# Optimization experiments

Measured on AMD Instinct MI355X. Metric: run time of the kernel, lower is better.

## Reference

```python
import jax, jax.numpy as jnp
import numpy as np

TOP_K = 50  # standard DND neighbourhood size
N_STEPS = 5


def _mlp(x, W1, b1, W2, b2, W3, b3):
    h = jax.nn.elu(x @ W1 + b1)
    h = jax.nn.elu(h @ W2 + b2)
    return h @ W3 + b3  # [B, 1]


def setup_inputs() -> dict:
    key = jax.random.key(0)
    ks = jax.random.split(key, 10)
    B, A, N, D = 1024, 5, 16384, 512
    return {
        "embeddings": jax.random.normal(ks[0], (B, D), jnp.float32),
        "keys": jax.random.normal(ks[1], (A, N, D), jnp.float32),
        "mem_values": jax.random.normal(ks[2], (A, N, D), jnp.float32),
        "W1": jax.random.normal(ks[3], (D, 256), jnp.float32) * 0.02,
        "b1": jnp.zeros((256,), jnp.float32),
        "W2": jax.random.normal(ks[4], (256, 128), jnp.float32) * 0.02,
        "b2": jnp.zeros((128,), jnp.float32),
        "W3": jax.random.normal(ks[5], (128, 1), jnp.float32) * 0.02,
        "b3": jnp.zeros((1,), jnp.float32),
        "actions": jax.random.randint(ks[6], (B, N_STEPS), 0, A, jnp.int32),
    }


def reference(embeddings, keys, mem_values, W1, b1, W2, b2, W3, b3, actions):
    # embeddings: [B, D]; keys/mem_values: [A, N, D]; actions: [B, 5]
    B, D = embeddings.shape
    eps = 1e-8
    # normalize memory keys once (cosine-similarity DND kernel)
    kn = keys / (jnp.linalg.norm(keys, axis=-1, keepdims=True) + eps)  # [A, N, D]

    def dnd_lookup_all(q):
        # q: [B, D] -> kNN-weighted readout from every action's memory: [A, B, D]
        qn = q / (jnp.linalg.norm(q, axis=-1, keepdims=True) + eps)
        sims = jnp.einsum("bd,and->abn", qn, kn)          # [A, B, N]
        s_k, idx = jax.lax.top_k(sims, TOP_K)             # [A, B, K]
        w = jax.nn.softmax(s_k, axis=-1)                  # [A, B, K]
        v_k = jax.vmap(lambda v, i: v[i])(mem_values, idx)  # [A, B, K, D]
        return jnp.einsum("abk,abkd->abd", w, v_k)

    pred_values = _mlp(embeddings, W1, b1, W2, b2, W3, b3)  # [B, 1]

    b_idx = jnp.arange(B)
    cur = embeddings
    step_vals = []
    for t in range(N_STEPS):
        out_all = dnd_lookup_all(cur)          # [A, B, D]
        cur = out_all[actions[:, t], b_idx]    # [B, D] per-sample action select
        step_vals.append(_mlp(cur, W1, b1, W2, b2, W3, b3))  # [B, 1]

    # original concatenates sample-major: [v1_i..v5_i] for each i -> [5B, 1]
    pred_nstep = jnp.stack(step_vals, axis=1).reshape(-1, 1)
    return jnp.concatenate([pred_values, pred_nstep], axis=0)  # [6B, 1]
```

## Files before the change

### kernel.cpp

```cpp
#include <hip/hip_runtime.h>

#define A_CNT   5
#define NB      1024
#define DIM     512
#define NMEM    16384
#define TOPK    50
#define NSTEPS  5
#define H1N     256
#define H2N     128

#define TM      128
#define TN      128
#define MSEL    100
#define RCAP    512

struct TileDesc { int a; int s0; int nvalid; int pad; };

typedef __bf16 bf16x8 __attribute__((ext_vector_type(8)));
typedef short  s16x8  __attribute__((ext_vector_type(8)));
typedef float  f32x4  __attribute__((ext_vector_type(4)));

template <typename T>
__device__ __forceinline__ auto mfma_try(T a, T b, f32x4 c, int)
    -> decltype(__builtin_amdgcn_mfma_f32_16x16x32_bf16(a, b, c, 0, 0, 0)) {
    return __builtin_amdgcn_mfma_f32_16x16x32_bf16(a, b, c, 0, 0, 0);
}
template <typename T>
__device__ __forceinline__ f32x4 mfma_try(T a, T b, f32x4 c, long) {
    return __builtin_amdgcn_mfma_f32_16x16x32_bf16(
        __builtin_bit_cast(s16x8, a), __builtin_bit_cast(s16x8, b), c, 0, 0, 0);
}
__device__ __forceinline__ f32x4 mfma_bf16(uint4 a, uint4 b, f32x4 c) {
    return mfma_try(__builtin_bit_cast(bf16x8, a), __builtin_bit_cast(bf16x8, b), c, 0);
}

union BF8 { bf16x8 v; uint4 u; };

__device__ __forceinline__ void gload_lds16(const void* g, void* l) {
    __builtin_amdgcn_global_load_lds(
        (const __attribute__((address_space(1))) void*)(unsigned long long)g,
        (__attribute__((address_space(3))) void*)(unsigned)(unsigned long long)l,
        16, 0, 0);
}

__global__ __launch_bounds__(256) void k_prep_keys(const float* __restrict__ keys,
                                                   float* __restrict__ inv,
                                                   unsigned short* __restrict__ kb) {
    int row  = blockIdx.x * 4 + (threadIdx.x >> 6);
    int lane = threadIdx.x & 63;
    const float* p = keys + (size_t)row * DIM;
    float ss = 0.f;
    for (int i = lane; i < DIM; i += 64) { float v = p[i]; ss += v * v; }
    for (int o = 32; o; o >>= 1) ss += __shfl_down(ss, o);
    ss = __shfl(ss, 0);
    if (lane == 0) inv[row] = 1.0f / (sqrtf(ss) + 1e-8f);
    const float4* s4 = (const float4*)(p + lane * 8);
    float4 v0 = s4[0], v1 = s4[1];
    BF8 pk;
    pk.v[0] = (__bf16)v0.x; pk.v[1] = (__bf16)v0.y;
    pk.v[2] = (__bf16)v0.z; pk.v[3] = (__bf16)v0.w;
    pk.v[4] = (__bf16)v1.x; pk.v[5] = (__bf16)v1.y;
    pk.v[6] = (__bf16)v1.z; pk.v[7] = (__bf16)v1.w;
    *(uint4*)(kb + (size_t)row * DIM + lane * 8) = pk.u;
}

__global__ __launch_bounds__(256) void k_qnorm(const float* __restrict__ x,
                                               float* __restrict__ qn,
                                               unsigned short* __restrict__ qb) {
    int row = blockIdx.x, tid = threadIdx.x;
    const float* p = x + (size_t)row * DIM;
    float ss = 0.f;
    for (int i = tid; i < DIM; i += 256) { float v = p[i]; ss += v * v; }
    for (int o = 32; o; o >>= 1) ss += __shfl_down(ss, o);
    __shared__ float w4[4];
    if ((tid & 63) == 0) w4[tid >> 6] = ss;
    __syncthreads();
    float tot = w4[0] + w4[1] + w4[2] + w4[3];
    float s = 1.0f / (sqrtf(tot) + 1e-8f);
    float* q = qn + (size_t)row * DIM;
    unsigned short* qbr = qb + (size_t)row * DIM;
    for (int i = tid; i < DIM; i += 256) {
        float v = p[i] * s;
        q[i] = v;
        __bf16 h = (__bf16)v;
        qbr[i] = __builtin_bit_cast(unsigned short, h);
    }
}

__global__ void k_group_all(const int* __restrict__ actions,
                            int* __restrict__ sorted_b_all, int* __restrict__ sorted_a_all,
                            TileDesc* __restrict__ descs_all, int cb, int maxd, int nch) {
    int t = blockIdx.x;
    int* sorted_b = sorted_b_all + t * NB;
    int* sorted_a = sorted_a_all + t * NB;
    TileDesc* descs = descs_all + t * (nch * maxd);
    int lane = threadIdx.x;
    for (int i = lane; i < nch * maxd; i += 64) descs[i].a = -1;
    __shared__ int gs[A_CNT + 1];
    int out_pos = 0;
    for (int a = 0; a < A_CNT; a++) {
        if (lane == 0) gs[a] = out_pos;
        for (int c = 0; c < NB; c += 64) {
            int b = c + lane;
            int act = actions[b * NSTEPS + t];
            unsigned long long m = __ballot(act == a);
            int rank = __popcll(m & ((1ULL << lane) - 1ULL));
            if (act == a) { sorted_b[out_pos + rank] = b; sorted_a[out_pos + rank] = a; }
            out_pos += __popcll(m);
        }
    }
    if (lane == 0) {
        gs[A_CNT] = NB;
        int ndc[4] = {0, 0, 0, 0};
        for (int a = 0; a < A_CNT; a++) {
            int s = gs[a], e = gs[a + 1];
            while (s < e) {
                int c = s / cb;
                int lim = min(e, (c + 1) * cb);
                int len = min(TM, lim - s);
                TileDesc d; d.a = a; d.s0 = s; d.nvalid = len; d.pad = 0;
                descs[c * maxd + ndc[c]++] = d;
                s += len;
            }
        }
    }
}

__global__ __launch_bounds__(256) void k_screen(
    const unsigned short* __restrict__ qb, const unsigned short* __restrict__ kb,
    const float* __restrict__ inv_kn, const int* __restrict__ sorted_b,
    const TileDesc* __restrict__ descs, int chunk_row0,
    unsigned short* __restrict__ simsb) {
    TileDesc d = descs[blockIdx.x];
    if (d.a < 0) return;
    int tid = threadIdx.x;
    int n0 = blockIdx.y * TN;
    __shared__ __align__(16) unsigned short Qs[TM][32];
    __shared__ __align__(16) unsigned short Ks[TN][32];
    __shared__ int rows[TM];
    if (tid < TM) rows[tid] = sorted_b[d.s0 + min(tid, d.nvalid - 1)];
    __syncthreads();

    int w = tid >> 6, lane = tid & 63;
    int g = lane >> 4, r15 = lane & 15;
    int wq = w >> 1, wn = w & 1;
    int swc = (g ^ ((r15 >> 1) & 3)) * 8;

    int srow = tid >> 2, schunk = ((tid & 3) ^ ((tid >> 3) & 3)) * 8;
    const unsigned short* kbase = kb + (size_t)d.a * NMEM * DIM;
    const unsigned short* q0 = qb + (size_t)rows[srow] * DIM + schunk;
    const unsigned short* q1 = qb + (size_t)rows[64 + srow] * DIM + schunk;
    const unsigned short* k0p = kbase + (size_t)(n0 + srow) * DIM + schunk;
    const unsigned short* k1p = kbase + (size_t)(n0 + 64 + srow) * DIM + schunk;
    char* ldsQ = (char*)&Qs[0][0] + tid * 16;
    char* ldsK = (char*)&Ks[0][0] + tid * 16;

    f32x4 acc[4][4];
#pragma unroll
    for (int i = 0; i < 4; i++)
#pragma unroll
        for (int j = 0; j < 4; j++) acc[i][j] = (f32x4){0.f, 0.f, 0.f, 0.f};

    for (int k0 = 0; k0 < DIM; k0 += 32) {
        gload_lds16(q0 + k0,  ldsQ);
        gload_lds16(q1 + k0,  ldsQ + 4096);
        gload_lds16(k0p + k0, ldsK);
        gload_lds16(k1p + k0, ldsK + 4096);
        __syncthreads();
        uint4 kf[4], qf[4];
#pragma unroll
        for (int m = 0; m < 4; m++)
            kf[m] = *(const uint4*)&Ks[wn * 64 + m * 16 + r15][swc];
#pragma unroll
        for (int m = 0; m < 4; m++)
            qf[m] = *(const uint4*)&Qs[wq * 64 + m * 16 + r15][swc];
#pragma unroll
        for (int i = 0; i < 4; i++)
#pragma unroll
            for (int j = 0; j < 4; j++)
                acc[i][j] = mfma_bf16(kf[i], qf[j], acc[i][j]);
        __syncthreads();
    }

    int sbase = d.s0 - chunk_row0;
#pragma unroll
    for (int j = 0; j < 4; j++) {
        int q = wq * 64 + j * 16 + r15;
        if (q < d.nvalid) {
            unsigned short* orow = simsb + (size_t)(sbase + q) * NMEM + n0;
#pragma unroll
            for (int i = 0; i < 4; i++) {
                int nb = wn * 64 + i * 16 + g * 4;
                float4 iv = *(const float4*)(inv_kn + (size_t)d.a * NMEM + n0 + nb);
                __bf16 e0 = (__bf16)(acc[i][j][0] * iv.x);
                __bf16 e1 = (__bf16)(acc[i][j][1] * iv.y);
                __bf16 e2 = (__bf16)(acc[i][j][2] * iv.z);
                __bf16 e3 = (__bf16)(acc[i][j][3] * iv.w);
                ushort4 o;
                o.x = __builtin_bit_cast(unsigned short, e0);
                o.y = __builtin_bit_cast(unsigned short, e1);
                o.z = __builtin_bit_cast(unsigned short, e2);
                o.w = __builtin_bit_cast(unsigned short, e3);
                *(ushort4*)(orow + nb) = o;
            }
        }
    }
}

__global__ __launch_bounds__(256) void k_topk(
    const unsigned short* __restrict__ simsb,
    const int* __restrict__ sorted_b, const int* __restrict__ sorted_a,
    int chunk_row0,
    const float* __restrict__ qn, const float* __restrict__ keys,
    const float* __restrict__ inv_kn,
    const float* __restrict__ memv, float* __restrict__ cur_next,
    float* __restrict__ qn_out, unsigned short* __restrict__ qb_out) {
    int tid = threadIdx.x;
    int s = chunk_row0 + blockIdx.x;
    int b = sorted_b[s], a = sorted_a[s];
    const unsigned short* row = simsb + (size_t)blockIdx.x * NMEM;

    __shared__ unsigned cnum;
    __shared__ int   cidx[RCAP];
    __shared__ float cval[RCAP];
    __shared__ __align__(16) float qs[DIM];
    __shared__ float selw[TOPK];
    __shared__ int   seli[TOPK];
    __shared__ int   wred[2][4];
    __shared__ float w4[4];

    uint4 rr[8];
#pragma unroll
    for (int c = 0; c < 8; c++) {
        uint4 v = ((const uint4*)row)[c * 256 + tid];
        unsigned s0 = (v.x >> 15) & 0x00010001u;
        unsigned s1 = (v.y >> 15) & 0x00010001u;
        unsigned s2 = (v.z >> 15) & 0x00010001u;
        unsigned s3 = (v.w >> 15) & 0x00010001u;
        v.x ^= 0x80008000u | (s0 * 0x7FFFu);
        v.y ^= 0x80008000u | (s1 * 0x7FFFu);
        v.z ^= 0x80008000u | (s2 * 0x7FFFu);
        v.w ^= 0x80008000u | (s3 * 0x7FFFu);
        rr[c] = v;
    }

    qs[tid]       = qn[(size_t)b * DIM + tid];
    qs[tid + 256] = qn[(size_t)b * DIM + tid + 256];
    if (tid == 0) cnum = 0;

    unsigned lo = 0, hi = 65536;
    for (int it = 0; it < 16; ++it) {
        unsigned mid = (lo + hi) >> 1;
        int cnt = 0;
#pragma unroll
        for (int c = 0; c < 8; c++) {
            unsigned w0 = rr[c].x, w1 = rr[c].y, w2 = rr[c].z, w3 = rr[c].w;
            cnt += ((w0 & 0xFFFFu) >= mid) + ((w0 >> 16) >= mid);
            cnt += ((w1 & 0xFFFFu) >= mid) + ((w1 >> 16) >= mid);
            cnt += ((w2 & 0xFFFFu) >= mid) + ((w2 >> 16) >= mid);
            cnt += ((w3 & 0xFFFFu) >= mid) + ((w3 >> 16) >= mid);
        }
        for (int o = 32; o; o >>= 1) cnt += __shfl_down(cnt, o);
        if ((tid & 63) == 0) wred[it & 1][tid >> 6] = cnt;
        __syncthreads();
        int tot = wred[it & 1][0] + wred[it & 1][1] + wred[it & 1][2] + wred[it & 1][3];
        if ((unsigned)tot >= MSEL) lo = mid; else hi = mid;
    }
    unsigned tau16 = lo;

#pragma unroll
    for (int c = 0; c < 8; c++) {
        unsigned uu[4] = {rr[c].x, rr[c].y, rr[c].z, rr[c].w};
#pragma unroll
        for (int q2 = 0; q2 < 4; q2++) {
#pragma unroll
            for (int hh = 0; hh < 2; hh++) {
                unsigned u16v = hh ? (uu[q2] >> 16) : (uu[q2] & 0xFFFFu);
                if (u16v >= tau16) {
                    unsigned p = atomicAdd(&cnum, 1u);
                    if (p < RCAP) cidx[p] = (c * 256 + tid) * 8 + q2 * 2 + hh;
                }
            }
        }
    }
    __syncthreads();
    int ncand = (int)cnum; if (ncand > RCAP) ncand = RCAP;

    const float* kbase = keys + (size_t)a * NMEM * DIM;
    const float* invp  = inv_kn + (size_t)a * NMEM;
    for (int i = tid; i < ncand; i += 256) {
        int n = cidx[i];
        const float4* kr = (const float4*)(kbase + (size_t)n * DIM);
        float acc = 0.f;
#pragma unroll 8
        for (int k4 = 0; k4 < DIM / 4; k4++) {
            float4 v = kr[k4];
            float4 qv = *(const float4*)&qs[k4 * 4];
            acc = fmaf(qv.x, v.x, acc);
            acc = fmaf(qv.y, v.y, acc);
            acc = fmaf(qv.z, v.z, acc);
            acc = fmaf(qv.w, v.w, acc);
        }
        cval[i] = acc * invp[n];
    }
    __syncthreads();

    for (int i = tid; i < ncand; i += 256) {
        float si = cval[i]; int ni = cidx[i];
        int rank = 0;
        for (int j = 0; j < ncand; j++) {
            float sj = cval[j];
            rank += (sj > si) || (sj == si && cidx[j] < ni);
        }
        if (rank < TOPK) { selw[rank] = si; seli[rank] = ni; }
    }
    __syncthreads();
    if (tid == 0) {
        float mx = selw[0];
        for (int i = 1; i < TOPK; i++) mx = fmaxf(mx, selw[i]);
        float ssum = 0.f;
        for (int i = 0; i < TOPK; i++) { float e = expf(selw[i] - mx); selw[i] = e; ssum += e; }
        float inv = 1.0f / ssum;
        for (int i = 0; i < TOPK; i++) selw[i] *= inv;
    }
    __syncthreads();

    const float* mv = memv + (size_t)a * NMEM * DIM;
    float acc0 = 0.f, acc1 = 0.f;
#pragma unroll 10
    for (int i = 0; i < TOPK; i++) {
        const float* vr = mv + (size_t)seli[i] * DIM;
        float wgt = selw[i];
        acc0 += wgt * vr[tid];
        acc1 += wgt * vr[tid + 256];
    }
    float* o = cur_next + (size_t)b * DIM;
    o[tid] = acc0;
    o[tid + 256] = acc1;

    float ss = 0.f;
    { float v = acc0; ss += v * v; }
    { float v = acc1; ss += v * v; }
    for (int o2 = 32; o2; o2 >>= 1) ss += __shfl_down(ss, o2);
    if ((tid & 63) == 0) w4[tid >> 6] = ss;
    __syncthreads();
    float tot = w4[0] + w4[1] + w4[2] + w4[3];
    float sc = 1.0f / (sqrtf(tot) + 1e-8f);
    float v0 = acc0 * sc, v1 = acc1 * sc;
    qn_out[(size_t)b * DIM + tid]       = v0;
    qn_out[(size_t)b * DIM + tid + 256] = v1;
    __bf16 h0 = (__bf16)v0, h1 = (__bf16)v1;
    qb_out[(size_t)b * DIM + tid]       = __builtin_bit_cast(unsigned short, h0);
    qb_out[(size_t)b * DIM + tid + 256] = __builtin_bit_cast(unsigned short, h1);
}

__global__ __launch_bounds__(256) void k_mlp_all(
    const float* __restrict__ emb, const float* __restrict__ steps,
    const float* __restrict__ W1, const float* __restrict__ b1,
    const float* __restrict__ W2, const float* __restrict__ b2,
    const float* __restrict__ W3, const float* __restrict__ b3,
    float* __restrict__ out) {
    int w = threadIdx.x >> 6, lane = threadIdx.x & 63;
    int r = blockIdx.x * 4 + w;
    const float* xr;
    int oidx;
    if (r < NB) {
        xr = emb + (size_t)r * DIM;
        oidx = r;
    } else {
        int rr = r - NB;
        int t = rr / NB, b = rr - t * NB;
        xr = steps + (size_t)rr * DIM;
        oidx = NB + b * NSTEPS + t;
    }
    __shared__ float xs[4][DIM];
    __shared__ float h1s[4][H1N];
#pragma unroll
    for (int i = 0; i < 2; i++) {
        float4 v = *(const float4*)(xr + (lane + i * 64) * 4);
        *(float4*)&xs[w][(lane + i * 64) * 4] = v;
    }
    __syncthreads();
    float a0 = b1[lane], a1 = b1[lane + 64], a2 = b1[lane + 128], a3 = b1[lane + 192];
    for (int k = 0; k < DIM; k++) {
        float xv = xs[w][k];
        const float* wr = W1 + k * H1N;
        a0 += xv * wr[lane];
        a1 += xv * wr[lane + 64];
        a2 += xv * wr[lane + 128];
        a3 += xv * wr[lane + 192];
    }
    h1s[w][lane]       = (a0 > 0.f) ? a0 : expm1f(a0);
    h1s[w][lane + 64]  = (a1 > 0.f) ? a1 : expm1f(a1);
    h1s[w][lane + 128] = (a2 > 0.f) ? a2 : expm1f(a2);
    h1s[w][lane + 192] = (a3 > 0.f) ? a3 : expm1f(a3);
    __syncthreads();
    float c0 = b2[lane], c1 = b2[lane + 64];
    for (int k = 0; k < H1N; k++) {
        float hv = h1s[w][k];
        c0 += hv * W2[k * H2N + lane];
        c1 += hv * W2[k * H2N + lane + 64];
    }
    c0 = ((c0 > 0.f) ? c0 : expm1f(c0)) * W3[lane];
    c1 = ((c1 > 0.f) ? c1 : expm1f(c1)) * W3[lane + 64];
    float ssum = c0 + c1;
    for (int o = 32; o; o >>= 1) ssum += __shfl_down(ssum, o);
    if (lane == 0) out[oidx] = ssum + b3[0];
}

extern "C" void kernel_launch(void* const* d_in, const int* in_sizes, int n_in,
                              void* d_out, int out_size, void* d_ws, size_t ws_size,
                              hipStream_t stream) {
    const float* emb  = (const float*)d_in[0];
    const float* keys = (const float*)d_in[1];
    const float* memv = (const float*)d_in[2];
    const float* W1 = (const float*)d_in[3];
    const float* b1 = (const float*)d_in[4];
    const float* W2 = (const float*)d_in[5];
    const float* b2 = (const float*)d_in[6];
    const float* W3 = (const float*)d_in[7];
    const float* b3 = (const float*)d_in[8];
    const int* actions = (const int*)d_in[9];
    float* out = (float*)d_out;

    char* ws = (char*)d_ws;
    size_t off = 0;
    auto alloc = [&](size_t bytes) -> void* {
        void* p = ws + off;
        off = (off + bytes + 255) & ~(size_t)255;
        return p;
    };
    float* inv_kn  = (float*)alloc(sizeof(float) * A_CNT * NMEM);
    float* qnA     = (float*)alloc(sizeof(float) * NB * DIM);
    float* qnB     = (float*)alloc(sizeof(float) * NB * DIM);
    unsigned short* qbA = (unsigned short*)alloc(sizeof(unsigned short) * NB * DIM);
    unsigned short* qbB = (unsigned short*)alloc(sizeof(unsigned short) * NB * DIM);
    unsigned short* kb = (unsigned short*)alloc(sizeof(unsigned short) * (size_t)A_CNT * NMEM * DIM);
    float* curAll  = (float*)alloc(sizeof(float) * (size_t)NSTEPS * NB * DIM);
    int* sorted_b  = (int*)alloc(sizeof(int) * NSTEPS * NB);
    int* sorted_a  = (int*)alloc(sizeof(int) * NSTEPS * NB);
    TileDesc* descs = (TileDesc*)alloc(sizeof(TileDesc) * 64 * NSTEPS);
    size_t rem = (ws_size > off) ? (ws_size - off) : 0;
    int CB = 256;
    if (rem >= sizeof(unsigned short) * (size_t)1024 * NMEM + 4096) CB = 1024;
    else if (rem >= sizeof(unsigned short) * (size_t)512 * NMEM + 4096) CB = 512;
    unsigned short* simsb = (unsigned short*)alloc(sizeof(unsigned short) * (size_t)CB * NMEM);
    int nch = NB / CB;
    int maxd = CB / TM + A_CNT;

    k_prep_keys<<<dim3(A_CNT * NMEM / 4), dim3(256), 0, stream>>>(keys, inv_kn, kb);
    k_group_all<<<dim3(NSTEPS), dim3(64), 0, stream>>>(actions, sorted_b, sorted_a, descs, CB, maxd, nch);
    k_qnorm<<<dim3(NB), dim3(256), 0, stream>>>(emb, qnA, qbA);

    float* qn_cur = qnA;  unsigned short* qb_cur = qbA;
    float* qn_nxt = qnB;  unsigned short* qb_nxt = qbB;
    for (int t = 0; t < NSTEPS; t++) {
        const int* sb = sorted_b + t * NB;
        const int* sa = sorted_a + t * NB;
        TileDesc* dsc = descs + t * (nch * maxd);
        float* nxt = curAll + (size_t)t * NB * DIM;
        for (int c = 0; c < nch; c++) {
            k_screen<<<dim3(maxd, NMEM / TN), dim3(256), 0, stream>>>(
                qb_cur, kb, inv_kn, sb, dsc + c * maxd, c * CB, simsb);
            k_topk<<<dim3(CB), dim3(256), 0, stream>>>(
                simsb, sb, sa, c * CB, qn_cur, keys, inv_kn, memv, nxt, qn_nxt, qb_nxt);
        }
        { float* tf = qn_cur; qn_cur = qn_nxt; qn_nxt = tf; }
        { unsigned short* ts = qb_cur; qb_cur = qb_nxt; qb_nxt = ts; }
    }
    k_mlp_all<<<dim3(6 * NB / 4), dim3(256), 0, stream>>>(
        emb, curAll, W1, b1, W2, b2, W3, b3, out);
}
```

Before: 1.057 ms.

## Replace per-row MLP kernel with tiled FP32 GEMM kernels plus final dot

The MLP over all 6B rows previously ran one wavefront per row, each streaming W1 and W2 from global memory. It now runs as register-blocked 128x128 shared-memory-tiled GEMMs with fused bias and ELU for layers 1 and 2, followed by a small dot-product kernel for the output layer. This increases weight reuse and arithmetic intensity. In exchange it adds intermediate H1/H2 buffers written to global memory and three extra launches.

```diff
diff --git a/kernel.cpp b/kernel.cpp
--- a/kernel.cpp
+++ b/kernel.cpp
@@ -354,55 +354,84 @@
     qb_out[(size_t)b * DIM + tid + 256] = __builtin_bit_cast(unsigned short, h1);
 }
 
-__global__ __launch_bounds__(256) void k_mlp_all(
-    const float* __restrict__ emb, const float* __restrict__ steps,
-    const float* __restrict__ W1, const float* __restrict__ b1,
-    const float* __restrict__ W2, const float* __restrict__ b2,
+__global__ __launch_bounds__(256) void k_mlp_gemm(
+    const float* __restrict__ x, int ldx,
+    const float* __restrict__ w,
+    const float* __restrict__ bias,
+    float* __restrict__ y, int N, int K) {
+    int m0 = blockIdx.x * 128;
+    int n0 = blockIdx.y * 128;
+    int tid = threadIdx.x;
+    __shared__ __align__(16) float As[32][132];
+    __shared__ __align__(16) float Bs[32][132];
+    int ty = tid >> 4, tx = tid & 15;
+    float acc[8][8];
+#pragma unroll
+    for (int j = 0; j < 8; j++) {
+        int cc = (j < 4) ? (tx * 4 + j) : (64 + tx * 4 + (j - 4));
+        float bv = bias[n0 + cc];
+#pragma unroll
+        for (int i = 0; i < 8; i++) acc[i][j] = bv;
+    }
+    for (int k0 = 0; k0 < K; k0 += 32) {
+#pragma unroll
+        for (int i = 0; i < 4; i++) {
+            int f4 = tid + i * 256;
+            int r = f4 >> 3;
+            int kq = (f4 & 7) * 4;
+            float4 v = *(const float4*)(x + (size_t)(m0 + r) * ldx + k0 + kq);
+            As[kq + 0][r] = v.x; As[kq + 1][r] = v.y;
+            As[kq + 2][r] = v.z; As[kq + 3][r] = v.w;
+        }
+#pragma unroll
+        for (int i = 0; i < 4; i++) {
+            int f4 = tid + i * 256;
+            int kk = f4 >> 5;
+            int n4 = (f4 & 31) * 4;
+            float4 v = *(const float4*)(w + (size_t)(k0 + kk) * N + n0 + n4);
+            Bs[kk][n4 + 0] = v.x; Bs[kk][n4 + 1] = v.y;
+            Bs[kk][n4 + 2] = v.z; Bs[kk][n4 + 3] = v.w;
+        }
+        __syncthreads();
+#pragma unroll
+        for (int k = 0; k < 32; k++) {
+            float4 a0 = *(const float4*)&As[k][ty * 4];
+            float4 a1 = *(const float4*)&As[k][64 + ty * 4];
+            float4 b0 = *(const float4*)&Bs[k][tx * 4];
+            float4 b1v = *(const float4*)&Bs[k][64 + tx * 4];
+            float ar[8] = {a0.x, a0.y, a0.z, a0.w, a1.x, a1.y, a1.z, a1.w};
+            float br[8] = {b0.x, b0.y, b0.z, b0.w, b1v.x, b1v.y, b1v.z, b1v.w};
+#pragma unroll
+            for (int i = 0; i < 8; i++)
+#pragma unroll
+                for (int j = 0; j < 8; j++) acc[i][j] += ar[i] * br[j];
+        }
+        __syncthreads();
+    }
+#pragma unroll
+    for (int i = 0; i < 8; i++) {
+        int r = m0 + ((i < 4) ? (ty * 4 + i) : (64 + ty * 4 + (i - 4)));
+        float* orow = y + (size_t)r * N + n0;
+#pragma unroll
+        for (int j = 0; j < 8; j++) {
+            int cc = (j < 4) ? (tx * 4 + j) : (64 + tx * 4 + (j - 4));
+            float v = acc[i][j];
+            orow[cc] = (v > 0.f) ? v : expm1f(v);
+        }
+    }
+}
+
+__global__ __launch_bounds__(256) void k_mlp_dot(
+    const float* __restrict__ h2e,
     const float* __restrict__ W3, const float* __restrict__ b3,
     float* __restrict__ out) {
     int w = threadIdx.x >> 6, lane = threadIdx.x & 63;
     int r = blockIdx.x * 4 + w;
-    const float* xr;
     int oidx;
-    if (r < NB) {
-        xr = emb + (size_t)r * DIM;
-        oidx = r;
-    } else {
-        int rr = r - NB;
-        int t = rr / NB, b = rr - t * NB;
-        xr = steps + (size_t)rr * DIM;
-        oidx = NB + b * NSTEPS + t;
-    }
-    __shared__ float xs[4][DIM];
-    __shared__ float h1s[4][H1N];
-#pragma unroll
-    for (int i = 0; i < 2; i++) {
-        float4 v = *(const float4*)(xr + (lane + i * 64) * 4);
-        *(float4*)&xs[w][(lane + i * 64) * 4] = v;
-    }
-    __syncthreads();
-    float a0 = b1[lane], a1 = b1[lane + 64], a2 = b1[lane + 128], a3 = b1[lane + 192];
-    for (int k = 0; k < DIM; k++) {
-        float xv = xs[w][k];
-        const float* wr = W1 + k * H1N;
-        a0 += xv * wr[lane];
-        a1 += xv * wr[lane + 64];
-        a2 += xv * wr[lane + 128];
-        a3 += xv * wr[lane + 192];
-    }
-    h1s[w][lane]       = (a0 > 0.f) ? a0 : expm1f(a0);
-    h1s[w][lane + 64]  = (a1 > 0.f) ? a1 : expm1f(a1);
-    h1s[w][lane + 128] = (a2 > 0.f) ? a2 : expm1f(a2);
-    h1s[w][lane + 192] = (a3 > 0.f) ? a3 : expm1f(a3);
-    __syncthreads();
-    float c0 = b2[lane], c1 = b2[lane + 64];
-    for (int k = 0; k < H1N; k++) {
-        float hv = h1s[w][k];
-        c0 += hv * W2[k * H2N + lane];
-        c1 += hv * W2[k * H2N + lane + 64];
-    }
-    c0 = ((c0 > 0.f) ? c0 : expm1f(c0)) * W3[lane];
-    c1 = ((c1 > 0.f) ? c1 : expm1f(c1)) * W3[lane + 64];
+    if (r < NB) oidx = r;
+    else { int rr = r - NB; int t = rr / NB, b = rr - t * NB; oidx = NB + b * NSTEPS + t; }
+    float c0 = h2e[(size_t)r * H2N + lane]      * W3[lane];
+    float c1 = h2e[(size_t)r * H2N + lane + 64] * W3[lane + 64];
     float ssum = c0 + c1;
     for (int o = 32; o; o >>= 1) ssum += __shfl_down(ssum, o);
     if (lane == 0) out[oidx] = ssum + b3[0];
@@ -437,6 +466,8 @@
     unsigned short* qbB = (unsigned short*)alloc(sizeof(unsigned short) * NB * DIM);
     unsigned short* kb = (unsigned short*)alloc(sizeof(unsigned short) * (size_t)A_CNT * NMEM * DIM);
     float* curAll  = (float*)alloc(sizeof(float) * (size_t)NSTEPS * NB * DIM);
+    float* H1      = (float*)alloc(sizeof(float) * (size_t)6 * NB * H1N);
+    float* H2      = (float*)alloc(sizeof(float) * (size_t)6 * NB * H2N);
     int* sorted_b  = (int*)alloc(sizeof(int) * NSTEPS * NB);
     int* sorted_a  = (int*)alloc(sizeof(int) * NSTEPS * NB);
     TileDesc* descs = (TileDesc*)alloc(sizeof(TileDesc) * 64 * NSTEPS);
@@ -468,6 +499,11 @@
         { float* tf = qn_cur; qn_cur = qn_nxt; qn_nxt = tf; }
         { unsigned short* ts = qb_cur; qb_cur = qb_nxt; qb_nxt = ts; }
     }
-    k_mlp_all<<<dim3(6 * NB / 4), dim3(256), 0, stream>>>(
-        emb, curAll, W1, b1, W2, b2, W3, b3, out);
-}
+    k_mlp_gemm<<<dim3(NB / 128, H1N / 128), dim3(256), 0, stream>>>(
+        emb, DIM, W1, b1, H1, H1N, DIM);
+    k_mlp_gemm<<<dim3(NSTEPS * NB / 128, H1N / 128), dim3(256), 0, stream>>>(
+        curAll, DIM, W1, b1, H1 + (size_t)NB * H1N, H1N, DIM);
+    k_mlp_gemm<<<dim3(6 * NB / 128, H2N / 128), dim3(256), 0, stream>>>(
+        H1, H1N, W2, b2, H2, H2N, H1N);
+    k_mlp_dot<<<dim3(6 * NB / 4), dim3(256), 0, stream>>>(H2, W3, b3, out);
+}
```

Result: slower. 1.108 ms (+4.9%).
